# Optimization experiments

Measured on AMD Instinct MI355X. Metric: run time of the kernel, lower is better.

## Reference

```python
import jax, jax.numpy as jnp
import numpy as np

B, S, D, H, F = 2, 2048, 1024, 16, 4096
DH = D // H


def setup_inputs() -> dict:
    key = jax.random.key(0)
    ks = jax.random.split(key, 8)
    scale = 0.02
    def nrm(k, shape):
        return jax.random.normal(k, shape, jnp.float32) * scale
    return {
        "x": jax.random.normal(ks[0], (B, S, D), jnp.float32),
        "ln1_g": jnp.ones((D,), jnp.float32),
        "ln1_b": jnp.zeros((D,), jnp.float32),
        "wq": nrm(ks[1], (D, D)), "bq": jnp.zeros((D,), jnp.float32),
        "wk": nrm(ks[2], (D, D)), "bk": jnp.zeros((D,), jnp.float32),
        "wv": nrm(ks[3], (D, D)), "bv": jnp.zeros((D,), jnp.float32),
        "wo": nrm(ks[4], (D, D)), "bo": jnp.zeros((D,), jnp.float32),
        "ln2_g": jnp.ones((D,), jnp.float32),
        "ln2_b": jnp.zeros((D,), jnp.float32),
        "w1": nrm(ks[5], (D, F)), "b1": jnp.zeros((F,), jnp.float32),
        "w2": nrm(ks[6], (F, D)), "b2": jnp.zeros((D,), jnp.float32),
    }


def _layernorm(x, g, b, eps=1e-5):
    m = jnp.mean(x, axis=-1, keepdims=True)
    v = jnp.var(x, axis=-1, keepdims=True)
    return (x - m) / jnp.sqrt(v + eps) * g + b


def reference(x, ln1_g, ln1_b, wq, bq, wk, bk, wv, bv, wo, bo,
              ln2_g, ln2_b, w1, b1, w2, b2):
    # GPT2Block forward, prefill path (state=None): K/V = ln_1(x), causal mask.
    Bx, Sx, Dx = x.shape
    h = _layernorm(x, ln1_g, ln1_b)

    def heads(t):  # [B,S,D] -> [B,H,S,DH]
        return t.reshape(Bx, Sx, H, DH).transpose(0, 2, 1, 3)

    q = heads(h @ wq + bq)
    k = heads(h @ wk + bk)
    v = heads(h @ wv + bv)

    scores = jnp.einsum('bhqd,bhkd->bhqk', q, k) / jnp.sqrt(jnp.float32(DH))
    # masked_softmax: key position < valid_len (= query_pos+1) kept; else -1e6
    causal = jnp.arange(Sx)[None, :] <= jnp.arange(Sx)[:, None]  # [S,S]
    scores = jnp.where(causal, scores, jnp.float32(-1e6))
    attn_w = jax.nn.softmax(scores, axis=-1)

    o = jnp.einsum('bhqk,bhkd->bhqd', attn_w, v)
    o = o.transpose(0, 2, 1, 3).reshape(Bx, Sx, Dx)
    attn_out = o @ wo + bo

    add1 = x + attn_out  # dropout inactive (eval)
    h2 = _layernorm(add1, ln2_g, ln2_b)
    mlp = jax.nn.gelu(h2 @ w1 + b1, approximate=False) @ w2 + b2
    return add1 + mlp
```

## Files before the change

### kernel.cpp

```cpp
#include <hip/hip_runtime.h>
#include <hip/hip_bf16.h>


#define BDIM 1024
#define SEQ 2048
#define NH 16
#define DHEAD 64
#define FDIM 4096
#define QKVD 3072

typedef __attribute__((ext_vector_type(8))) short short8v;
typedef __attribute__((ext_vector_type(4))) float floatx4;

__device__ __forceinline__ unsigned short f2bf(float f) {
    unsigned int u = __float_as_uint(f);
    unsigned int r = u + 0x7FFFu + ((u >> 16) & 1u);
    return (unsigned short)(r >> 16);
}
__device__ __forceinline__ unsigned int pack2bf(float a, float b) {
    return (unsigned int)f2bf(a) | ((unsigned int)f2bf(b) << 16);
}

__device__ __forceinline__ void load16_lds(const unsigned short* g, short* l) {
    __builtin_amdgcn_global_load_lds((const __attribute__((address_space(1))) void*)g,
                                     (__attribute__((address_space(3))) void*)l, 16, 0, 0);
}

__global__ __launch_bounds__(256) void transpose_bf16(const float* __restrict__ W,
                                                      unsigned short* __restrict__ Wt,
                                                      int K, int N) {
    __shared__ float tile[32][33];
    const int t = threadIdx.x;
    const int r = t >> 3, c4 = (t & 7) * 4;
    const int n0 = blockIdx.x * 32, k0 = blockIdx.y * 32;
    float4 p = *(const float4*)(W + (size_t)(k0 + r) * N + n0 + c4);
    tile[r][c4 + 0] = p.x;
    tile[r][c4 + 1] = p.y;
    tile[r][c4 + 2] = p.z;
    tile[r][c4 + 3] = p.w;
    __syncthreads();
    ushort4 ou;
    ou.x = f2bf(tile[c4 + 0][r]);
    ou.y = f2bf(tile[c4 + 1][r]);
    ou.z = f2bf(tile[c4 + 2][r]);
    ou.w = f2bf(tile[c4 + 3][r]);
    *(ushort4*)(Wt + (size_t)(n0 + r) * K + k0 + c4) = ou;
}

__global__ void concat_bias(const float* __restrict__ a, const float* __restrict__ b,
                            const float* __restrict__ c, float* __restrict__ out) {
    int i = blockIdx.x * 256 + threadIdx.x;
    out[i] = (i < 1024) ? a[i] : (i < 2048 ? b[i - 1024] : c[i - 2048]);
}

__global__ __launch_bounds__(256) void transpose_v(const unsigned short* __restrict__ qkv,
                                                   unsigned short* __restrict__ vt) {
    const int bh = blockIdx.y;
    const int b = bh >> 4, h = bh & 15;
    const int s0 = blockIdx.x * 64;
    __shared__ unsigned short tile[64][80];
    const int t = threadIdx.x;
#pragma unroll
    for (int j = 0; j < 2; ++j) {
        const int c = j * 256 + t;
        const int s = c >> 3, d8 = (c & 7) * 8;
        uint4 p = *(const uint4*)(qkv + (size_t)(b * SEQ + s0 + s) * QKVD + 2048 + h * 64 + d8);
        *(uint4*)&tile[s][d8] = p;
    }
    __syncthreads();
#pragma unroll
    for (int j = 0; j < 2; ++j) {
        const int c = j * 256 + t;
        const int d = c >> 3, s8 = (c & 7) * 8;
        unsigned int w0 = (unsigned int)tile[s8 + 0][d] | ((unsigned int)tile[s8 + 1][d] << 16);
        unsigned int w1 = (unsigned int)tile[s8 + 2][d] | ((unsigned int)tile[s8 + 3][d] << 16);
        unsigned int w2 = (unsigned int)tile[s8 + 4][d] | ((unsigned int)tile[s8 + 5][d] << 16);
        unsigned int w3 = (unsigned int)tile[s8 + 6][d] | ((unsigned int)tile[s8 + 7][d] << 16);
        uint4 o = {w0, w1, w2, w3};
        *(uint4*)(vt + ((size_t)bh * 64 + d) * SEQ + s0 + s8) = o;
    }
}

__global__ __launch_bounds__(256) void ln_kernel(const float* __restrict__ x,
                                                 const float* __restrict__ g,
                                                 const float* __restrict__ bb,
                                                 unsigned short* __restrict__ out) {
    const int row = blockIdx.x;
    const int t = threadIdx.x;
    const int c = t * 4;
    float4 p = *(const float4*)(x + (size_t)row * BDIM + c);
    float s = p.x + p.y + p.z + p.w;
    float sq = p.x * p.x + p.y * p.y + p.z * p.z + p.w * p.w;
    for (int off = 1; off < 64; off <<= 1) {
        s += __shfl_xor(s, off);
        sq += __shfl_xor(sq, off);
    }
    __shared__ float ssum[4], ssq[4];
    const int wave = t >> 6, lane = t & 63;
    if (lane == 0) { ssum[wave] = s; ssq[wave] = sq; }
    __syncthreads();
    s = ssum[0] + ssum[1] + ssum[2] + ssum[3];
    sq = ssq[0] + ssq[1] + ssq[2] + ssq[3];
    const float mean = s * (1.0f / BDIM);
    const float var = sq * (1.0f / BDIM) - mean * mean;
    const float rstd = rsqrtf(var + 1e-5f);
    float4 gg = *(const float4*)(g + c);
    float4 bv = *(const float4*)(bb + c);
    ushort4 o;
    o.x = f2bf((p.x - mean) * rstd * gg.x + bv.x);
    o.y = f2bf((p.y - mean) * rstd * gg.y + bv.y);
    o.z = f2bf((p.z - mean) * rstd * gg.z + bv.z);
    o.w = f2bf((p.w - mean) * rstd * gg.w + bv.w);
    *(ushort4*)(out + (size_t)row * BDIM + c) = o;
}

template <int BN, int RES, int GELU, int OBF16, int QSCALE = 0>
__global__ __launch_bounds__(256, 3) void mfma_gemm(const unsigned short* __restrict__ A,
                                                    const unsigned short* __restrict__ Bt,
                                                    const float* __restrict__ bias,
                                                    const float* __restrict__ res,
                                                    void* __restrict__ Cv,
                                                    int M, int N, int K) {
    constexpr int MI = (BN == 128) ? 4 : 2;
    constexpr int CHB = BN * 4;
    __shared__ short As[2][128 * 32];
    __shared__ short Bs[2][BN * 32];
    const int t = threadIdx.x;
    const int wave = t >> 6, lane = t & 63;
    const int m0 = blockIdx.y * 128, n0 = blockIdx.x * BN;
    const int wmrow = (BN == 128) ? (wave & 1) * 64 : wave * 32;
    const int wnrow = (BN == 128) ? (wave >> 1) * 64 : 0;
    const int mlane = lane & 15, quad = lane >> 4;

    floatx4 acc[MI][4];
#pragma unroll
    for (int mi = 0; mi < MI; ++mi)
#pragma unroll
        for (int ni = 0; ni < 4; ++ni) {
            floatx4 z = {0.0f, 0.0f, 0.0f, 0.0f};
            acc[mi][ni] = z;
        }

    for (int k0 = 0; k0 < K; k0 += 64) {
        __syncthreads();
#pragma unroll
        for (int j = 0; j < 4; ++j) {
            const int c = j * 256 + t;
            const int hh = c >> 9, cc = c & 511;
            load16_lds(A + (size_t)(m0 + (cc >> 2)) * K + k0 + hh * 32 + (cc & 3) * 8,
                       &As[hh][cc * 8]);
        }
#pragma unroll
        for (int j = 0; j < CHB / 128; ++j) {
            const int c = j * 256 + t;
            const int hh = c / CHB, cc = c % CHB;
            load16_lds(Bt + (size_t)(n0 + (cc >> 2)) * K + k0 + hh * 32 + (cc & 3) * 8,
                       &Bs[hh][cc * 8]);
        }
        __syncthreads();
#pragma unroll
        for (int hh = 0; hh < 2; ++hh) {
            short8v a[MI], b[4];
#pragma unroll
            for (int mi = 0; mi < MI; ++mi)
                a[mi] = *(const short8v*)&As[hh][(wmrow + mi * 16 + mlane) * 32 + quad * 8];
#pragma unroll
            for (int ni = 0; ni < 4; ++ni)
                b[ni] = *(const short8v*)&Bs[hh][(wnrow + ni * 16 + mlane) * 32 + quad * 8];
#pragma unroll
            for (int mi = 0; mi < MI; ++mi)
#pragma unroll
                for (int ni = 0; ni < 4; ++ni)
                    acc[mi][ni] = __builtin_amdgcn_mfma_f32_16x16x32_bf16(a[mi], b[ni], acc[mi][ni], 0, 0, 0);
        }
    }
#pragma unroll
    for (int mi = 0; mi < MI; ++mi) {
#pragma unroll
        for (int ni = 0; ni < 4; ++ni) {
            const int col = n0 + wnrow + ni * 16 + mlane;
            const float bv = bias[col];
#pragma unroll
            for (int rg = 0; rg < 4; ++rg) {
                const int row = m0 + wmrow + mi * 16 + quad * 4 + rg;
                float v = acc[mi][ni][rg] + bv;
                if (RES) v += res[(size_t)row * N + col];
                if (GELU) v = 0.5f * v * (1.0f + erff(v * 0.70710678118654752f));
                if (QSCALE && col < 1024) v *= 0.125f;
                if (OBF16)
                    ((unsigned short*)Cv)[(size_t)row * N + col] = f2bf(v);
                else
                    ((float*)Cv)[(size_t)row * N + col] = v;
            }
        }
    }
}

__global__ __launch_bounds__(256) void attn_kernel(const unsigned short* __restrict__ qkv,
                                                   const unsigned short* __restrict__ vt,
                                                   unsigned short* __restrict__ o) {
    const int b = blockIdx.z, h = blockIdx.y;
    const int qt = b ? (int)(gridDim.x - 1 - blockIdx.x) : (int)blockIdx.x;
    const int t = threadIdx.x;
    const int wave = t >> 6, lane = t & 63;
    const int mlane = lane & 15, quad = lane >> 4;
    const int wq0 = qt * 128 + wave * 32;
    const size_t bS = (size_t)b * SEQ;

    __shared__ unsigned short Ks[32][72];
    __shared__ unsigned short Vs[64][40];
    __shared__ __align__(16) unsigned short plds[4][2][16][40];

    short8v qf[2][2];
#pragma unroll
    for (int ng = 0; ng < 2; ++ng) {
        const unsigned short* qrow = qkv + (bS + wq0 + ng * 16 + mlane) * QKVD + h * DHEAD;
        qf[ng][0] = *(const short8v*)(qrow + quad * 8);
        qf[ng][1] = *(const short8v*)(qrow + 32 + quad * 8);
    }

    const unsigned short* kbase = qkv + bS * QKVD + 1024 + h * DHEAD;
    const unsigned short* vbase = vt + ((size_t)(b * NH + h)) * DHEAD * SEQ;

    const int kr = t >> 3, ko = (t & 7) * 8;
    const int vd = t >> 2, vo = (t & 3) * 8;
    const unsigned short* kg = kbase + (size_t)kr * QKVD + ko;
    const unsigned short* vg = vbase + (size_t)vd * SEQ + vo;

    floatx4 ot[2][4];
#pragma unroll
    for (int ng = 0; ng < 2; ++ng)
#pragma unroll
        for (int mt = 0; mt < 4; ++mt) { floatx4 z = {0, 0, 0, 0}; ot[ng][mt] = z; }
    float m_r[2] = {-INFINITY, -INFINITY}, l_r[2] = {0.0f, 0.0f};

    const int kend = wq0 + 32;
    const int kmax = qt * 128 + 128;

    uint4 kreg = *(const uint4*)kg;
    uint4 vreg = *(const uint4*)vg;

    for (int k0 = 0; k0 < kmax; k0 += 32) {
        *(uint4*)&Ks[kr][ko] = kreg;
        *(uint4*)&Vs[vd][vo] = vreg;
        __syncthreads();
        if (k0 + 32 < kmax) {
            kreg = *(const uint4*)(kg + (size_t)(k0 + 32) * QKVD);
            vreg = *(const uint4*)(vg + (k0 + 32));
        }
        if (k0 < kend) {
            short8v kf[2][2], vf[4];
#pragma unroll
            for (int kt = 0; kt < 2; ++kt) {
                kf[kt][0] = *(const short8v*)&Ks[kt * 16 + mlane][quad * 8];
                kf[kt][1] = *(const short8v*)&Ks[kt * 16 + mlane][32 + quad * 8];
            }
#pragma unroll
            for (int mt = 0; mt < 4; ++mt)
                vf[mt] = *(const short8v*)&Vs[mt * 16 + mlane][quad * 8];

            floatx4 st[2][2];
#pragma unroll
            for (int ng = 0; ng < 2; ++ng)
#pragma unroll
                for (int kt = 0; kt < 2; ++kt) {
                    floatx4 z = {0, 0, 0, 0};
                    st[ng][kt] = __builtin_amdgcn_mfma_f32_16x16x32_bf16(kf[kt][0], qf[ng][0], z, 0, 0, 0);
                    st[ng][kt] = __builtin_amdgcn_mfma_f32_16x16x32_bf16(kf[kt][1], qf[ng][1], st[ng][kt], 0, 0, 0);
                }

            if (k0 == wq0) {
#pragma unroll
                for (int ng = 0; ng < 2; ++ng)
#pragma unroll
                    for (int kt = 0; kt < 2; ++kt)
#pragma unroll
                        for (int rg = 0; rg < 4; ++rg)
                            if (k0 + kt * 16 + quad * 4 + rg > wq0 + ng * 16 + mlane)
                                st[ng][kt][rg] = -1e30f;
            }

#pragma unroll
            for (int ng = 0; ng < 2; ++ng) {
                float tm = st[ng][0][0];
#pragma unroll
                for (int kt = 0; kt < 2; ++kt)
#pragma unroll
                    for (int rg = 0; rg < 4; ++rg) tm = fmaxf(tm, st[ng][kt][rg]);
                tm = fmaxf(tm, __shfl_xor(tm, 16));
                tm = fmaxf(tm, __shfl_xor(tm, 32));
                const float newm = fmaxf(m_r[ng], tm);
                const float alpha = __expf(m_r[ng] - newm);
                m_r[ng] = newm;
                float p[2][4], psum = 0.0f;
#pragma unroll
                for (int kt = 0; kt < 2; ++kt)
#pragma unroll
                    for (int rg = 0; rg < 4; ++rg) {
                        p[kt][rg] = __expf(st[ng][kt][rg] - newm);
                        psum += p[kt][rg];
                    }
                psum += __shfl_xor(psum, 16);
                psum += __shfl_xor(psum, 32);
                l_r[ng] = l_r[ng] * alpha + psum;
#pragma unroll
                for (int mt = 0; mt < 4; ++mt)
#pragma unroll
                    for (int rg = 0; rg < 4; ++rg) ot[ng][mt][rg] *= alpha;
#pragma unroll
                for (int kt = 0; kt < 2; ++kt) {
                    uint2 pk;
                    pk.x = pack2bf(p[kt][0], p[kt][1]);
                    pk.y = pack2bf(p[kt][2], p[kt][3]);
                    *(uint2*)&plds[wave][ng][mlane][kt * 16 + quad * 4] = pk;
                }
            }

#pragma unroll
            for (int ng = 0; ng < 2; ++ng) {
                short8v pf = *(const short8v*)&plds[wave][ng][mlane][quad * 8];
#pragma unroll
                for (int mt = 0; mt < 4; ++mt)
                    ot[ng][mt] = __builtin_amdgcn_mfma_f32_16x16x32_bf16(vf[mt], pf, ot[ng][mt], 0, 0, 0);
            }
        }
        __syncthreads();
    }

#pragma unroll
    for (int ng = 0; ng < 2; ++ng) {
        const float inv = 1.0f / l_r[ng];
        unsigned short* orow = o + (bS + wq0 + ng * 16 + mlane) * BDIM + h * DHEAD;
#pragma unroll
        for (int mt = 0; mt < 4; ++mt) {
            uint2 pk;
            pk.x = pack2bf(ot[ng][mt][0] * inv, ot[ng][mt][1] * inv);
            pk.y = pack2bf(ot[ng][mt][2] * inv, ot[ng][mt][3] * inv);
            *(uint2*)(orow + mt * 16 + quad * 4) = pk;
        }
    }
}

extern "C" void kernel_launch(void* const* d_in, const int* in_sizes, int n_in,
                              void* d_out, int out_size, void* d_ws, size_t ws_size,
                              hipStream_t stream) {
    const int M = 2 * SEQ;

    const float* x = (const float*)d_in[0];
    const float* ln1_g = (const float*)d_in[1];
    const float* ln1_b = (const float*)d_in[2];
    const float* wq = (const float*)d_in[3];
    const float* bq = (const float*)d_in[4];
    const float* wk = (const float*)d_in[5];
    const float* bk = (const float*)d_in[6];
    const float* wv = (const float*)d_in[7];
    const float* bv = (const float*)d_in[8];
    const float* wo = (const float*)d_in[9];
    const float* bo = (const float*)d_in[10];
    const float* ln2_g = (const float*)d_in[11];
    const float* ln2_b = (const float*)d_in[12];
    const float* w1 = (const float*)d_in[13];
    const float* b1 = (const float*)d_in[14];
    const float* w2 = (const float*)d_in[15];
    const float* b2 = (const float*)d_in[16];

    char* wsb = (char*)d_ws;
    unsigned short* qkv = (unsigned short*)wsb;
    unsigned short* ffn = (unsigned short*)wsb;
    unsigned short* vt = (unsigned short*)(wsb + (24u << 20));
    unsigned short* hbuf = (unsigned short*)(wsb + (32u << 20));
    float* add1 = (float*)(wsb + (40u << 20));
    unsigned short* h2 = (unsigned short*)(wsb + (56u << 20));
    unsigned short* qkvT = (unsigned short*)(wsb + (64u << 20));
    unsigned short* woT = (unsigned short*)(wsb + (70u << 20));
    unsigned short* w1T = (unsigned short*)(wsb + (72u << 20));
    unsigned short* w2T = (unsigned short*)(wsb + (80u << 20));
    float* bqkv = (float*)(wsb + (88u << 20));

    transpose_bf16<<<dim3(32, 32), 256, 0, stream>>>(wq, qkvT, 1024, 1024);
    transpose_bf16<<<dim3(32, 32), 256, 0, stream>>>(wk, qkvT + 1024 * 1024, 1024, 1024);
    transpose_bf16<<<dim3(32, 32), 256, 0, stream>>>(wv, qkvT + 2048 * 1024, 1024, 1024);
    transpose_bf16<<<dim3(32, 32), 256, 0, stream>>>(wo, woT, 1024, 1024);
    transpose_bf16<<<dim3(128, 32), 256, 0, stream>>>(w1, w1T, 1024, 4096);
    transpose_bf16<<<dim3(32, 128), 256, 0, stream>>>(w2, w2T, 4096, 1024);
    concat_bias<<<12, 256, 0, stream>>>(bq, bk, bv, bqkv);

    ln_kernel<<<M, 256, 0, stream>>>(x, ln1_g, ln1_b, hbuf);

    mfma_gemm<128, 0, 0, 1, 1><<<dim3(QKVD / 128, M / 128), 256, 0, stream>>>(
        hbuf, qkvT, bqkv, nullptr, qkv, M, QKVD, 1024);

    transpose_v<<<dim3(SEQ / 64, 32), 256, 0, stream>>>(qkv, vt);

    attn_kernel<<<dim3(SEQ / 128, NH, 2), 256, 0, stream>>>(qkv, vt, hbuf);

    mfma_gemm<64, 1, 0, 0><<<dim3(1024 / 64, M / 128), 256, 0, stream>>>(
        hbuf, woT, bo, x, add1, M, 1024, 1024);

    ln_kernel<<<M, 256, 0, stream>>>(add1, ln2_g, ln2_b, h2);

    mfma_gemm<128, 0, 1, 1><<<dim3(FDIM / 128, M / 128), 256, 0, stream>>>(
        h2, w1T, b1, nullptr, ffn, M, FDIM, 1024);

    mfma_gemm<64, 1, 0, 0><<<dim3(1024 / 64, M / 128), 256, 0, stream>>>(
        ffn, w2T, b2, add1, (float*)d_out, M, 1024, FDIM);
}
```

Before: 376.2 us.

## Merge weight transposes, fuse V transpose into QKV GEMM, widen attention key tiles

Replaces six weight-transpose launches with a single flattened launch. Drops the separate V-transpose kernel by having the QKV GEMM epilogue write V directly in transposed [b,h,d,s] layout. Widens the attention kernel's key/value tile from 32 to 64 keys per iteration, with per-subtile causal skipping, and reorders the grid so the heaviest query tiles launch first. The aim is fewer launches, no extra pass over V, and fewer barriers per key. The costs are larger LDS use, more registers in attention, and uncoalesced 8-byte strided V stores in the GEMM epilogue.

```diff
diff --git a/kernel.cpp b/kernel.cpp
--- a/kernel.cpp
+++ b/kernel.cpp
@@ -26,13 +26,38 @@
                                      (__attribute__((address_space(3))) void*)l, 16, 0, 0);
 }
 
-__global__ __launch_bounds__(256) void transpose_bf16(const float* __restrict__ W,
-                                                      unsigned short* __restrict__ Wt,
-                                                      int K, int N) {
+__global__ __launch_bounds__(256) void transpose_all(const float* __restrict__ wq,
+                                                     const float* __restrict__ wk,
+                                                     const float* __restrict__ wv,
+                                                     const float* __restrict__ wo,
+                                                     const float* __restrict__ w1,
+                                                     const float* __restrict__ w2,
+                                                     unsigned short* __restrict__ qkvT,
+                                                     unsigned short* __restrict__ woT,
+                                                     unsigned short* __restrict__ w1T,
+                                                     unsigned short* __restrict__ w2T) {
+    const int g = blockIdx.x;
+    const float* W;
+    unsigned short* Wt;
+    int K, N, tx, ty;
+    if (g < 4096) {
+        const int w = g >> 10, tile = g & 1023;
+        tx = tile & 31; ty = tile >> 5; K = 1024; N = 1024;
+        W = (w == 0) ? wq : (w == 1) ? wk : (w == 2) ? wv : wo;
+        Wt = (w == 3) ? woT : qkvT + (size_t)w * 1024 * 1024;
+    } else if (g < 8192) {
+        const int tile = g - 4096;
+        tx = tile & 127; ty = tile >> 7; K = 1024; N = 4096;
+        W = w1; Wt = w1T;
+    } else {
+        const int tile = g - 8192;
+        tx = tile & 31; ty = tile >> 5; K = 4096; N = 1024;
+        W = w2; Wt = w2T;
+    }
     __shared__ float tile[32][33];
     const int t = threadIdx.x;
     const int r = t >> 3, c4 = (t & 7) * 4;
-    const int n0 = blockIdx.x * 32, k0 = blockIdx.y * 32;
+    const int n0 = tx * 32, k0 = ty * 32;
     float4 p = *(const float4*)(W + (size_t)(k0 + r) * N + n0 + c4);
     tile[r][c4 + 0] = p.x;
     tile[r][c4 + 1] = p.y;
@@ -51,34 +76,6 @@
                             const float* __restrict__ c, float* __restrict__ out) {
     int i = blockIdx.x * 256 + threadIdx.x;
     out[i] = (i < 1024) ? a[i] : (i < 2048 ? b[i - 1024] : c[i - 2048]);
-}
-
-__global__ __launch_bounds__(256) void transpose_v(const unsigned short* __restrict__ qkv,
-                                                   unsigned short* __restrict__ vt) {
-    const int bh = blockIdx.y;
-    const int b = bh >> 4, h = bh & 15;
-    const int s0 = blockIdx.x * 64;
-    __shared__ unsigned short tile[64][80];
-    const int t = threadIdx.x;
-#pragma unroll
-    for (int j = 0; j < 2; ++j) {
-        const int c = j * 256 + t;
-        const int s = c >> 3, d8 = (c & 7) * 8;
-        uint4 p = *(const uint4*)(qkv + (size_t)(b * SEQ + s0 + s) * QKVD + 2048 + h * 64 + d8);
-        *(uint4*)&tile[s][d8] = p;
-    }
-    __syncthreads();
-#pragma unroll
-    for (int j = 0; j < 2; ++j) {
-        const int c = j * 256 + t;
-        const int d = c >> 3, s8 = (c & 7) * 8;
-        unsigned int w0 = (unsigned int)tile[s8 + 0][d] | ((unsigned int)tile[s8 + 1][d] << 16);
-        unsigned int w1 = (unsigned int)tile[s8 + 2][d] | ((unsigned int)tile[s8 + 3][d] << 16);
-        unsigned int w2 = (unsigned int)tile[s8 + 4][d] | ((unsigned int)tile[s8 + 5][d] << 16);
-        unsigned int w3 = (unsigned int)tile[s8 + 6][d] | ((unsigned int)tile[s8 + 7][d] << 16);
-        uint4 o = {w0, w1, w2, w3};
-        *(uint4*)(vt + ((size_t)bh * 64 + d) * SEQ + s0 + s8) = o;
-    }
 }
 
 __global__ __launch_bounds__(256) void ln_kernel(const float* __restrict__ x,
@@ -114,12 +111,13 @@
     *(ushort4*)(out + (size_t)row * BDIM + c) = o;
 }
 
-template <int BN, int RES, int GELU, int OBF16, int QSCALE = 0>
+template <int BN, int RES, int GELU, int OBF16, int QSCALE = 0, int VOUT = 0>
 __global__ __launch_bounds__(256, 3) void mfma_gemm(const unsigned short* __restrict__ A,
                                                     const unsigned short* __restrict__ Bt,
                                                     const float* __restrict__ bias,
                                                     const float* __restrict__ res,
                                                     void* __restrict__ Cv,
+                                                    unsigned short* __restrict__ vtout,
                                                     int M, int N, int K) {
     constexpr int MI = (BN == 128) ? 4 : 2;
     constexpr int CHB = BN * 4;
@@ -180,17 +178,27 @@
         for (int ni = 0; ni < 4; ++ni) {
             const int col = n0 + wnrow + ni * 16 + mlane;
             const float bv = bias[col];
-#pragma unroll
-            for (int rg = 0; rg < 4; ++rg) {
-                const int row = m0 + wmrow + mi * 16 + quad * 4 + rg;
-                float v = acc[mi][ni][rg] + bv;
-                if (RES) v += res[(size_t)row * N + col];
-                if (GELU) v = 0.5f * v * (1.0f + erff(v * 0.70710678118654752f));
-                if (QSCALE && col < 1024) v *= 0.125f;
-                if (OBF16)
-                    ((unsigned short*)Cv)[(size_t)row * N + col] = f2bf(v);
-                else
-                    ((float*)Cv)[(size_t)row * N + col] = v;
+            const int row0 = m0 + wmrow + mi * 16 + quad * 4;
+            if (VOUT && col >= 2048) {
+                const int vd = col - 2048;
+                const int bb = row0 >> 11, ss = row0 & 2047;
+                uint2 pk;
+                pk.x = pack2bf(acc[mi][ni][0] + bv, acc[mi][ni][1] + bv);
+                pk.y = pack2bf(acc[mi][ni][2] + bv, acc[mi][ni][3] + bv);
+                *(uint2*)(vtout + ((size_t)(bb * NH + (vd >> 6)) * DHEAD + (vd & 63)) * SEQ + ss) = pk;
+            } else {
+#pragma unroll
+                for (int rg = 0; rg < 4; ++rg) {
+                    const int row = row0 + rg;
+                    float v = acc[mi][ni][rg] + bv;
+                    if (RES) v += res[(size_t)row * N + col];
+                    if (GELU) v = 0.5f * v * (1.0f + erff(v * 0.70710678118654752f));
+                    if (QSCALE && col < 1024) v *= 0.125f;
+                    if (OBF16)
+                        ((unsigned short*)Cv)[(size_t)row * N + col] = f2bf(v);
+                    else
+                        ((float*)Cv)[(size_t)row * N + col] = v;
+                }
             }
         }
     }
@@ -199,17 +207,19 @@
 __global__ __launch_bounds__(256) void attn_kernel(const unsigned short* __restrict__ qkv,
                                                    const unsigned short* __restrict__ vt,
                                                    unsigned short* __restrict__ o) {
-    const int b = blockIdx.z, h = blockIdx.y;
-    const int qt = b ? (int)(gridDim.x - 1 - blockIdx.x) : (int)blockIdx.x;
+    const int g = blockIdx.x;
+    const int qt = (g < 256) ? (15 - (g >> 5)) : ((g - 256) >> 5);
+    const int hb = g & 31;
+    const int h = hb & 15, b = hb >> 4;
     const int t = threadIdx.x;
     const int wave = t >> 6, lane = t & 63;
     const int mlane = lane & 15, quad = lane >> 4;
     const int wq0 = qt * 128 + wave * 32;
     const size_t bS = (size_t)b * SEQ;
 
-    __shared__ unsigned short Ks[32][72];
-    __shared__ unsigned short Vs[64][40];
-    __shared__ __align__(16) unsigned short plds[4][2][16][40];
+    __shared__ unsigned short Ks[64][72];
+    __shared__ unsigned short Vs[64][72];
+    __shared__ __align__(16) unsigned short plds[4][2][16][72];
 
     short8v qf[2][2];
 #pragma unroll
@@ -222,10 +232,11 @@
     const unsigned short* kbase = qkv + bS * QKVD + 1024 + h * DHEAD;
     const unsigned short* vbase = vt + ((size_t)(b * NH + h)) * DHEAD * SEQ;
 
-    const int kr = t >> 3, ko = (t & 7) * 8;
-    const int vd = t >> 2, vo = (t & 3) * 8;
-    const unsigned short* kg = kbase + (size_t)kr * QKVD + ko;
-    const unsigned short* vg = vbase + (size_t)vd * SEQ + vo;
+    const int sr = t >> 3, so = (t & 7) * 8;
+    const unsigned short* kg0 = kbase + (size_t)sr * QKVD + so;
+    const unsigned short* kg1 = kbase + (size_t)(32 + sr) * QKVD + so;
+    const unsigned short* vg0 = vbase + (size_t)sr * SEQ + so;
+    const unsigned short* vg1 = vbase + (size_t)(32 + sr) * SEQ + so;
 
     floatx4 ot[2][4];
 #pragma unroll
@@ -237,54 +248,60 @@
     const int kend = wq0 + 32;
     const int kmax = qt * 128 + 128;
 
-    uint4 kreg = *(const uint4*)kg;
-    uint4 vreg = *(const uint4*)vg;
-
-    for (int k0 = 0; k0 < kmax; k0 += 32) {
-        *(uint4*)&Ks[kr][ko] = kreg;
-        *(uint4*)&Vs[vd][vo] = vreg;
+    uint4 kr0 = *(const uint4*)kg0;
+    uint4 kr1 = *(const uint4*)kg1;
+    uint4 vr0 = *(const uint4*)vg0;
+    uint4 vr1 = *(const uint4*)vg1;
+
+    for (int k0 = 0; k0 < kmax; k0 += 64) {
+        *(uint4*)&Ks[sr][so] = kr0;
+        *(uint4*)&Ks[32 + sr][so] = kr1;
+        *(uint4*)&Vs[sr][so] = vr0;
+        *(uint4*)&Vs[32 + sr][so] = vr1;
         __syncthreads();
-        if (k0 + 32 < kmax) {
-            kreg = *(const uint4*)(kg + (size_t)(k0 + 32) * QKVD);
-            vreg = *(const uint4*)(vg + (k0 + 32));
+        if (k0 + 64 < kmax) {
+            kr0 = *(const uint4*)(kg0 + (size_t)(k0 + 64) * QKVD);
+            kr1 = *(const uint4*)(kg1 + (size_t)(k0 + 64) * QKVD);
+            vr0 = *(const uint4*)(vg0 + (k0 + 64));
+            vr1 = *(const uint4*)(vg1 + (k0 + 64));
         }
         if (k0 < kend) {
-            short8v kf[2][2], vf[4];
-#pragma unroll
-            for (int kt = 0; kt < 2; ++kt) {
-                kf[kt][0] = *(const short8v*)&Ks[kt * 16 + mlane][quad * 8];
-                kf[kt][1] = *(const short8v*)&Ks[kt * 16 + mlane][32 + quad * 8];
+            floatx4 st[2][4];
+#pragma unroll
+            for (int ng = 0; ng < 2; ++ng)
+#pragma unroll
+                for (int kt = 0; kt < 4; ++kt) {
+                    floatx4 mz = {-1e30f, -1e30f, -1e30f, -1e30f};
+                    st[ng][kt] = mz;
+                }
+#pragma unroll
+            for (int kt = 0; kt < 4; ++kt) {
+                if (k0 + kt * 16 < kend) {
+                    short8v kfa = *(const short8v*)&Ks[kt * 16 + mlane][quad * 8];
+                    short8v kfb = *(const short8v*)&Ks[kt * 16 + mlane][32 + quad * 8];
+#pragma unroll
+                    for (int ng = 0; ng < 2; ++ng) {
+                        floatx4 z = {0, 0, 0, 0};
+                        st[ng][kt] = __builtin_amdgcn_mfma_f32_16x16x32_bf16(kfa, qf[ng][0], z, 0, 0, 0);
+                        st[ng][kt] = __builtin_amdgcn_mfma_f32_16x16x32_bf16(kfb, qf[ng][1], st[ng][kt], 0, 0, 0);
+                    }
+                }
             }
-#pragma unroll
-            for (int mt = 0; mt < 4; ++mt)
-                vf[mt] = *(const short8v*)&Vs[mt * 16 + mlane][quad * 8];
-
-            floatx4 st[2][2];
-#pragma unroll
-            for (int ng = 0; ng < 2; ++ng)
-#pragma unroll
-                for (int kt = 0; kt < 2; ++kt) {
-                    floatx4 z = {0, 0, 0, 0};
-                    st[ng][kt] = __builtin_amdgcn_mfma_f32_16x16x32_bf16(kf[kt][0], qf[ng][0], z, 0, 0, 0);
-                    st[ng][kt] = __builtin_amdgcn_mfma_f32_16x16x32_bf16(kf[kt][1], qf[ng][1], st[ng][kt], 0, 0, 0);
-                }
-
-            if (k0 == wq0) {
+            if (k0 + 64 >= kend) {
 #pragma unroll
                 for (int ng = 0; ng < 2; ++ng)
 #pragma unroll
-                    for (int kt = 0; kt < 2; ++kt)
+                    for (int kt = 0; kt < 4; ++kt)
 #pragma unroll
                         for (int rg = 0; rg < 4; ++rg)
                             if (k0 + kt * 16 + quad * 4 + rg > wq0 + ng * 16 + mlane)
                                 st[ng][kt][rg] = -1e30f;
             }
-
 #pragma unroll
             for (int ng = 0; ng < 2; ++ng) {
                 float tm = st[ng][0][0];
 #pragma unroll
-                for (int kt = 0; kt < 2; ++kt)
+                for (int kt = 0; kt < 4; ++kt)
 #pragma unroll
                     for (int rg = 0; rg < 4; ++rg) tm = fmaxf(tm, st[ng][kt][rg]);
                 tm = fmaxf(tm, __shfl_xor(tm, 16));
@@ -292,9 +309,9 @@
                 const float newm = fmaxf(m_r[ng], tm);
                 const float alpha = __expf(m_r[ng] - newm);
                 m_r[ng] = newm;
-                float p[2][4], psum = 0.0f;
-#pragma unroll
-                for (int kt = 0; kt < 2; ++kt)
+                float p[4][4], psum = 0.0f;
+#pragma unroll
+                for (int kt = 0; kt < 4; ++kt)
 #pragma unroll
                     for (int rg = 0; rg < 4; ++rg) {
                         p[kt][rg] = __expf(st[ng][kt][rg] - newm);
@@ -308,20 +325,28 @@
 #pragma unroll
                     for (int rg = 0; rg < 4; ++rg) ot[ng][mt][rg] *= alpha;
 #pragma unroll
-                for (int kt = 0; kt < 2; ++kt) {
+                for (int kt = 0; kt < 4; ++kt) {
                     uint2 pk;
                     pk.x = pack2bf(p[kt][0], p[kt][1]);
                     pk.y = pack2bf(p[kt][2], p[kt][3]);
                     *(uint2*)&plds[wave][ng][mlane][kt * 16 + quad * 4] = pk;
                 }
             }
-
-#pragma unroll
-            for (int ng = 0; ng < 2; ++ng) {
-                short8v pf = *(const short8v*)&plds[wave][ng][mlane][quad * 8];
-#pragma unroll
-                for (int mt = 0; mt < 4; ++mt)
-                    ot[ng][mt] = __builtin_amdgcn_mfma_f32_16x16x32_bf16(vf[mt], pf, ot[ng][mt], 0, 0, 0);
+#pragma unroll
+            for (int kh = 0; kh < 2; ++kh) {
+                if (k0 + kh * 32 < kend) {
+                    short8v vf[4];
+#pragma unroll
+                    for (int mt = 0; mt < 4; ++mt)
+                        vf[mt] = *(const short8v*)&Vs[mt * 16 + mlane][kh * 32 + quad * 8];
+#pragma unroll
+                    for (int ng = 0; ng < 2; ++ng) {
+                        short8v pf = *(const short8v*)&plds[wave][ng][mlane][kh * 32 + quad * 8];
+#pragma unroll
+                        for (int mt = 0; mt < 4; ++mt)
+                            ot[ng][mt] = __builtin_amdgcn_mfma_f32_16x16x32_bf16(vf[mt], pf, ot[ng][mt], 0, 0, 0);
+                    }
+                }
             }
         }
         __syncthreads();
@@ -377,31 +402,24 @@
     unsigned short* w2T = (unsigned short*)(wsb + (80u << 20));
     float* bqkv = (float*)(wsb + (88u << 20));
 
-    transpose_bf16<<<dim3(32, 32), 256, 0, stream>>>(wq, qkvT, 1024, 1024);
-    transpose_bf16<<<dim3(32, 32), 256, 0, stream>>>(wk, qkvT + 1024 * 1024, 1024, 1024);
-    transpose_bf16<<<dim3(32, 32), 256, 0, stream>>>(wv, qkvT + 2048 * 1024, 1024, 1024);
-    transpose_bf16<<<dim3(32, 32), 256, 0, stream>>>(wo, woT, 1024, 1024);
-    transpose_bf16<<<dim3(128, 32), 256, 0, stream>>>(w1, w1T, 1024, 4096);
-    transpose_bf16<<<dim3(32, 128), 256, 0, stream>>>(w2, w2T, 4096, 1024);
+    transpose_all<<<12288, 256, 0, stream>>>(wq, wk, wv, wo, w1, w2, qkvT, woT, w1T, w2T);
     concat_bias<<<12, 256, 0, stream>>>(bq, bk, bv, bqkv);
 
     ln_kernel<<<M, 256, 0, stream>>>(x, ln1_g, ln1_b, hbuf);
 
-    mfma_gemm<128, 0, 0, 1, 1><<<dim3(QKVD / 128, M / 128), 256, 0, stream>>>(
-        hbuf, qkvT, bqkv, nullptr, qkv, M, QKVD, 1024);
-
-    transpose_v<<<dim3(SEQ / 64, 32), 256, 0, stream>>>(qkv, vt);
-
-    attn_kernel<<<dim3(SEQ / 128, NH, 2), 256, 0, stream>>>(qkv, vt, hbuf);
+    mfma_gemm<128, 0, 0, 1, 1, 1><<<dim3(QKVD / 128, M / 128), 256, 0, stream>>>(
+        hbuf, qkvT, bqkv, nullptr, qkv, vt, M, QKVD, 1024);
+
+    attn_kernel<<<512, 256, 0, stream>>>(qkv, vt, hbuf);
 
     mfma_gemm<64, 1, 0, 0><<<dim3(1024 / 64, M / 128), 256, 0, stream>>>(
-        hbuf, woT, bo, x, add1, M, 1024, 1024);
+        hbuf, woT, bo, x, add1, nullptr, M, 1024, 1024);
 
     ln_kernel<<<M, 256, 0, stream>>>(add1, ln2_g, ln2_b, h2);
 
     mfma_gemm<128, 0, 1, 1><<<dim3(FDIM / 128, M / 128), 256, 0, stream>>>(
-        h2, w1T, b1, nullptr, ffn, M, FDIM, 1024);
+        h2, w1T, b1, nullptr, ffn, nullptr, M, FDIM, 1024);
 
     mfma_gemm<64, 1, 0, 0><<<dim3(1024 / 64, M / 128), 256, 0, stream>>>(
-        ffn, w2T, b2, add1, (float*)d_out, M, 1024, FDIM);
-}
+        ffn, w2T, b2, add1, (float*)d_out, nullptr, M, 1024, FDIM);
+}
```

New measurement: 358.3 us. 4.8% less time.
